# Optimization experiments

Hardware: AMD Instinct MI355X
Metric: run time of the kernel (lower is better)

Reference implementation:

```python
import jax, jax.numpy as jnp
import numpy as np

# Dims: C = 8*8*4 = 256 input channels, O = 8*8*8 = 512 output channels,
# space_rank = 4, TT ranks = (4, 16, 16).

def setup_inputs() -> dict:
    key = jax.random.key(0)
    ks = jax.random.split(key, 6)
    inp = jax.random.normal(ks[0], (32, 256, 32, 32), dtype=jnp.float32)
    # space_factor: (space_rank, 1, kH, kW)
    space_factor = jax.random.normal(ks[1], (4, 1, 3, 3), dtype=jnp.float32) * 0.3
    # factors[i]: (in_i, rank_i, rank_{i+1}, out_i)
    factor0 = jax.random.normal(ks[2], (8, 4, 16, 8), dtype=jnp.float32) * 0.1
    factor1 = jax.random.normal(ks[3], (8, 16, 16, 8), dtype=jnp.float32) * 0.08
    # last_factor: (in_last, rank_last, out_last)
    last_factor = jax.random.normal(ks[4], (4, 16, 8), dtype=jnp.float32) * 0.1
    bias = jax.random.uniform(ks[5], (512,), dtype=jnp.float32, minval=-0.02, maxval=0.02)
    return {"input": inp, "space_factor": space_factor, "factor0": factor0,
            "factor1": factor1, "last_factor": last_factor, "bias": bias}


def reference(input, space_factor, factor0, factor1, last_factor, bias):
    B, C, H, W = input.shape
    sr = space_factor.shape[0]
    # Depthwise conv: each of the C channels convolved with the same
    # `space_rank` filters (torch repeat along out-channel dim + groups=C).
    w = jnp.tile(space_factor, (C, 1, 1, 1))  # (C*sr, 1, kH, kW)
    y = jax.lax.conv_general_dilated(
        input, w, window_strides=(1, 1), padding=[(1, 1), (1, 1)],
        feature_group_count=C,
        dimension_numbers=("NCHW", "OIHW", "NCHW"))  # (B, C*sr, H', W')
    Hp, Wp = y.shape[2], y.shape[3]
    # (B, n0, n1, n2, sr, H', W') with (n0,n1,n2) = input_chanel_shape
    t = y.reshape(B, 8, 8, 4, sr, Hp, Wp)
    # Contract the tiny TT cores first (optimal order found by tn.contractors.optimal):
    # chain: (n0, n1, n2, r0, o0, o1, o2) -- only ~0.5M elements.
    chain = jnp.einsum("apqx,bqry,crz->abcpxyz", factor0, factor1, last_factor)
    # One big contraction over (n0, n1, n2, r0): effectively a GEMM
    # (B*H'*W', C*sr) x (C*sr, O).
    out = jnp.einsum("nabcphw,abcpxyz->nxyzhw", t, chain)
    out = out.reshape(B, 512, Hp, Wp)
    return out + bias[None, :, None, None]
```

## Files before the change

### kernel.cpp

```cpp
#include <hip/hip_runtime.h>

typedef unsigned short ushort_t;
typedef __attribute__((ext_vector_type(8))) short bf16x8;
typedef __attribute__((ext_vector_type(4))) float f32x4;

__device__ __forceinline__ unsigned short f2bf(float f) {
  union { float f; unsigned u; } x; x.f = f;
  unsigned r = x.u + 0x7FFFu + ((x.u >> 16) & 1u);
  return (unsigned short)(r >> 16);
}

__global__ void chain_g_kernel(const float* __restrict__ f1,
                               const float* __restrict__ lf,
                               float* __restrict__ g) {
  int idx = blockIdx.x * 256 + threadIdx.x;
  int z = idx & 7, c = (idx >> 3) & 3, y = (idx >> 5) & 7,
      q = (idx >> 8) & 15, b = idx >> 12;
  float s = 0.f;
  #pragma unroll
  for (int r = 0; r < 16; ++r)
    s += f1[((b * 16 + q) * 16 + r) * 8 + y] * lf[(c * 16 + r) * 8 + z];
  g[idx] = s;
}

__global__ void chain_kernel(const float* __restrict__ f0,
                             const float* __restrict__ g,
                             ushort_t* __restrict__ chainT) {
  int idx = blockIdx.x * 256 + threadIdx.x;
  int k = idx & 1023, o = idx >> 10;
  int p = k & 3, c = (k >> 2) & 3, b = (k >> 4) & 7, a = k >> 7;
  int z = o & 7, y = (o >> 3) & 7, x = o >> 6;
  float s = 0.f;
  #pragma unroll
  for (int q = 0; q < 16; ++q)
    s += f0[((a * 4 + p) * 16 + q) * 8 + x] *
         g[(((b * 16 + q) * 8 + y) * 4 + c) * 8 + z];
  chainT[idx] = f2bf(s);
}

#define AS1 __attribute__((address_space(1)))
#define AS3 __attribute__((address_space(3)))
#define BARRIER  __builtin_amdgcn_s_barrier()
#define LGKMCNT0 asm volatile("s_waitcnt lgkmcnt(0)" ::: "memory")
#define VMCNT0   asm volatile("s_waitcnt vmcnt(0)" ::: "memory")

__global__ __launch_bounds__(512, 2) void fused_kernel(const float* __restrict__ in,
                                                       const float* __restrict__ sf,
                                                       const ushort_t* __restrict__ chainT,
                                                       const float* __restrict__ bias,
                                                       float* __restrict__ out) {
  __shared__ __align__(16) ushort_t Bs[512 * 64];
  __shared__ __align__(16) ushort_t As[128 * 64];
  __shared__ __align__(16) float Is[2][16][6][32];

  int tid = threadIdx.x;
  int bid = blockIdx.x;
  int wg = (bid & 7) * 32 + (bid >> 3);
  int n = wg >> 3, hq = wg & 7;
  int h0 = hq * 4;

  int lane = tid & 63, wv = tid >> 6;
  int wm = (wv >> 2) * 64, wn = (wv & 3) * 128;
  int lr = lane & 15, kg = lane >> 4;
  int kph0 = ((kg * 8) ^ ((lane & 7) * 8));
  int kph1 = ((32 + kg * 8) ^ ((lane & 7) * 8));

  int srow = tid >> 3;
  int scol = ((tid & 7) ^ (srow & 7)) * 8;
  const ushort_t* sB = chainT + (size_t)srow * 1024 + scol;
  int bdst = srow * 64 + (tid & 7) * 8;

  int cw = tid & 31, hp = (tid >> 5) & 1, ch2 = tid >> 6;

  float sfr[36];
  #pragma unroll
  for (int i = 0; i < 36; ++i)
    sfr[i] = __int_as_float(__builtin_amdgcn_readfirstlane(__float_as_int(sf[i])));

  float bv[8];
  #pragma unroll
  for (int nf = 0; nf < 8; ++nf) bv[nf] = bias[wn + nf * 16 + lr];

  f32x4 acc[4][8];
  #pragma unroll
  for (int i = 0; i < 4; ++i)
    #pragma unroll
    for (int j = 0; j < 8; ++j) acc[i][j] = (f32x4){0.f, 0.f, 0.f, 0.f};

  const float* inb = in + (size_t)n * 256 * 1024;

#define STAGE_IN(kt)                                                                          \
  _Pragma("unroll")                                                                           \
  for (int i = 0; i < 2; ++i) {                                                              \
    int e = tid + i * 512;                                                                   \
    if (e < 768) {                                                                           \
      int ch = e / 48, rem = e % 48, r = rem >> 3, w4 = rem & 7;                             \
      int hh = h0 - 1 + r;                                                                   \
      float4 v = make_float4(0.f, 0.f, 0.f, 0.f);                                            \
      if (hh >= 0 && hh < 32)                                                                \
        v = *(const float4*)&inb[(size_t)((kt) * 16 + ch) * 1024 + hh * 32 + w4 * 4];        \
      *(float4*)&Is[(kt) & 1][ch][r][w4 * 4] = v;                                            \
    }                                                                                        \
  }

#define STAGE_B(kt)                                                                           \
  _Pragma("unroll")                                                                           \
  for (int l = 0; l < 8; ++l)                                                                \
    __builtin_amdgcn_global_load_lds(                                                        \
        (const AS1 void*)(sB + (size_t)l * 65536 + (kt) * 64),                               \
        (AS3 void*)&Bs[l * 4096 + bdst], 16, 0, 0);

  STAGE_IN(0)
  LGKMCNT0; BARRIER;

  for (int kt = 0; kt < 16; ++kt) {
    if (kt < 15) { STAGE_IN(kt + 1) }
    STAGE_B(kt)
    {
      int ib = kt & 1;
      #pragma unroll
      for (int b = 0; b < 2; ++b) {
        int ch = ch2 * 2 + b;
        float v[4], mL[4], mR[4];
        #pragma unroll
        for (int r = 0; r < 4; ++r) {
          float x = Is[ib][ch][hp * 2 + r][cw];
          v[r] = x;
          float up = __shfl_up(x, 1);
          float dn = __shfl_down(x, 1);
          mL[r] = (cw == 0) ? 0.f : up;
          mR[r] = (cw == 31) ? 0.f : dn;
        }
        #pragma unroll
        for (int j = 0; j < 2; ++j) {
          float s[4];
          #pragma unroll
          for (int p = 0; p < 4; ++p) {
            float a_ = 0.f;
            #pragma unroll
            for (int dr = 0; dr < 3; ++dr) {
              a_ += mL[j + dr] * sfr[p * 9 + dr * 3 + 0];
              a_ += v[j + dr]  * sfr[p * 9 + dr * 3 + 1];
              a_ += mR[j + dr] * sfr[p * 9 + dr * 3 + 2];
            }
            s[p] = a_;
          }
          unsigned lo = (unsigned)f2bf(s[0]) | ((unsigned)f2bf(s[1]) << 16);
          unsigned hi = (unsigned)f2bf(s[2]) | ((unsigned)f2bf(s[3]) << 16);
          int row = (hp * 2 + j) * 32 + cw;
          uint2 pk; pk.x = lo; pk.y = hi;
          *(uint2*)&As[row * 64 + (ch2 ^ (cw & 7)) * 8 + b * 4] = pk;
        }
      }
    }
    LGKMCNT0; VMCNT0; BARRIER;

    #pragma unroll
    for (int ks = 0; ks < 2; ++ks) {
      int kph = ks ? kph1 : kph0;
      bf16x8 af[4];
      #pragma unroll
      for (int mf = 0; mf < 4; ++mf)
        af[mf] = *(const bf16x8*)&As[(wm + mf * 16 + lr) * 64 + kph];
      #pragma unroll
      for (int ng = 0; ng < 2; ++ng) {
        bf16x8 bf4[4];
        #pragma unroll
        for (int nq = 0; nq < 4; ++nq)
          bf4[nq] = *(const bf16x8*)&Bs[(wn + ng * 64 + nq * 16 + lr) * 64 + kph];
        __builtin_amdgcn_s_setprio(1);
        #pragma unroll
        for (int mf = 0; mf < 4; ++mf)
          #pragma unroll
          for (int nq = 0; nq < 4; ++nq)
            acc[mf][ng * 4 + nq] =
                __builtin_amdgcn_mfma_f32_16x16x32_bf16(af[mf], bf4[nq], acc[mf][ng * 4 + nq], 0, 0, 0);
        __builtin_amdgcn_s_setprio(0);
      }
    }
    LGKMCNT0; BARRIER;
  }
#undef STAGE_IN
#undef STAGE_B

  #pragma unroll
  for (int mf = 0; mf < 4; ++mf)
    #pragma unroll
    for (int nf = 0; nf < 8; ++nf) {
      int mloc = hq * 128 + wm + mf * 16 + kg * 4;
      int o = wn + nf * 16 + lr;
      f32x4 vv = acc[mf][nf];
      vv[0] += bv[nf]; vv[1] += bv[nf]; vv[2] += bv[nf]; vv[3] += bv[nf];
      *(f32x4*)&out[(size_t)n * 524288 + (size_t)o * 1024 + mloc] = vv;
    }
}

extern "C" void kernel_launch(void* const* d_in, const int* in_sizes, int n_in,
                              void* d_out, int out_size, void* d_ws, size_t ws_size,
                              hipStream_t stream) {
  (void)in_sizes; (void)n_in; (void)out_size; (void)ws_size;
  const float* in   = (const float*)d_in[0];
  const float* sf   = (const float*)d_in[1];
  const float* f0   = (const float*)d_in[2];
  const float* f1   = (const float*)d_in[3];
  const float* lf   = (const float*)d_in[4];
  const float* bias = (const float*)d_in[5];
  float* out = (float*)d_out;

  char* ws = (char*)d_ws;
  ushort_t* chainT = (ushort_t*)ws;
  float*    g      = (float*)(ws + 1048576);

  hipLaunchKernelGGL(chain_g_kernel, dim3(128),  dim3(256), 0, stream, f1, lf, g);
  hipLaunchKernelGGL(chain_kernel,   dim3(2048), dim3(256), 0, stream, f0, g, chainT);
  hipLaunchKernelGGL(fused_kernel,   dim3(256),  dim3(512), 0, stream, in, sf, chainT, bias, out);
}
```

Baseline: 76.70 us.

## Software-pipeline conv staging with MFMA via double-buffered A tile and register prefetch

Restructures the main K loop into a two-stage pipeline. The A tile is double-buffered so the depthwise conv for the next K step runs right after the MFMAs of the current one. Input loads are issued into registers two steps ahead and written to LDS later, with a partial vmcnt wait so global latency stays in flight. The conv now reads halo taps from padded LDS rows instead of using lane shuffles. This adds LDS use and barrier complexity, which may reduce occupancy.

```diff
diff --git a/kernel.cpp b/kernel.cpp
--- a/kernel.cpp
+++ b/kernel.cpp
@@ -42,6 +42,7 @@
 #define AS3 __attribute__((address_space(3)))
 #define BARRIER  __builtin_amdgcn_s_barrier()
 #define LGKMCNT0 asm volatile("s_waitcnt lgkmcnt(0)" ::: "memory")
+#define VMCNT3   asm volatile("s_waitcnt vmcnt(3)" ::: "memory")
 #define VMCNT0   asm volatile("s_waitcnt vmcnt(0)" ::: "memory")
 
 __global__ __launch_bounds__(512, 2) void fused_kernel(const float* __restrict__ in,
@@ -49,9 +50,9 @@
                                                        const ushort_t* __restrict__ chainT,
                                                        const float* __restrict__ bias,
                                                        float* __restrict__ out) {
-  __shared__ __align__(16) ushort_t Bs[512 * 64];
-  __shared__ __align__(16) ushort_t As[128 * 64];
-  __shared__ __align__(16) float Is[2][16][6][32];
+  __shared__ __align__(16) ushort_t Bs[32768];
+  __shared__ __align__(16) ushort_t As[2][8192];
+  __shared__ __align__(16) float Is[6528];
 
   int tid = threadIdx.x;
   int bid = blockIdx.x;
@@ -68,9 +69,25 @@
   int srow = tid >> 3;
   int scol = ((tid & 7) ^ (srow & 7)) * 8;
   const ushort_t* sB = chainT + (size_t)srow * 1024 + scol;
-  int bdst = srow * 64 + (tid & 7) * 8;
-
-  int cw = tid & 31, hp = (tid >> 5) & 1, ch2 = tid >> 6;
+
+  int cw = tid & 31, hp = (tid >> 5) & 1, ch2 = wv;
+  int clm = (cw == 0) ? 33 : cw - 1;
+  int crp = (cw == 31) ? 32 : cw + 1;
+  int aswz = (ch2 ^ (cw & 7)) * 8;
+
+  int isrc[3], ild[3], izer[3];
+  #pragma unroll
+  for (int i = 0; i < 3; ++i) {
+    int e = tid + i * 512;
+    int ch = e / 96, rem = e % 96, r = rem >> 4, w2 = rem & 15;
+    int hh = h0 - 1 + r;
+    int hcl = hh < 0 ? 0 : (hh > 31 ? 31 : hh);
+    izer[i] = (hh < 0) | (hh > 31);
+    isrc[i] = ch * 1024 + hcl * 32 + w2 * 2;
+    ild[i]  = ch * 204 + r * 34 + w2 * 2;
+  }
+  const float* inb = in + (size_t)n * 262144;
+  float2 rin[3];
 
   float sfr[36];
   #pragma unroll
@@ -87,101 +104,122 @@
     #pragma unroll
     for (int j = 0; j < 8; ++j) acc[i][j] = (f32x4){0.f, 0.f, 0.f, 0.f};
 
-  const float* inb = in + (size_t)n * 256 * 1024;
-
-#define STAGE_IN(kt)                                                                          \
-  _Pragma("unroll")                                                                           \
-  for (int i = 0; i < 2; ++i) {                                                              \
-    int e = tid + i * 512;                                                                   \
-    if (e < 768) {                                                                           \
-      int ch = e / 48, rem = e % 48, r = rem >> 3, w4 = rem & 7;                             \
-      int hh = h0 - 1 + r;                                                                   \
-      float4 v = make_float4(0.f, 0.f, 0.f, 0.f);                                            \
-      if (hh >= 0 && hh < 32)                                                                \
-        v = *(const float4*)&inb[(size_t)((kt) * 16 + ch) * 1024 + hh * 32 + w4 * 4];        \
-      *(float4*)&Is[(kt) & 1][ch][r][w4 * 4] = v;                                            \
-    }                                                                                        \
-  }
-
-#define STAGE_B(kt)                                                                           \
-  _Pragma("unroll")                                                                           \
-  for (int l = 0; l < 8; ++l)                                                                \
-    __builtin_amdgcn_global_load_lds(                                                        \
-        (const AS1 void*)(sB + (size_t)l * 65536 + (kt) * 64),                               \
-        (AS3 void*)&Bs[l * 4096 + bdst], 16, 0, 0);
-
-  STAGE_IN(0)
+#define ISSUE_IN(KT)                                                                     \
+  _Pragma("unroll")                                                                      \
+  for (int i = 0; i < 3; ++i)                                                            \
+    rin[i] = *(const float2*)&inb[(size_t)(KT) * 16384 + isrc[i]];
+
+#define WRITE_IN(IB)                                                                     \
+  _Pragma("unroll")                                                                      \
+  for (int i = 0; i < 3; ++i) {                                                          \
+    float2 v = rin[i];                                                                   \
+    if (izer[i]) { v.x = 0.f; v.y = 0.f; }                                               \
+    *(float2*)&Is[(IB) * 3264 + ild[i]] = v;                                             \
+  }
+
+#define STAGE_B(KT)                                                                      \
+  _Pragma("unroll")                                                                      \
+  for (int l = 0; l < 8; ++l)                                                            \
+    __builtin_amdgcn_global_load_lds(                                                    \
+        (const AS1 void*)(sB + (size_t)l * 65536 + (KT) * 64),                           \
+        (AS3 void*)&Bs[l * 4096 + tid * 8], 16, 0, 0);
+
+#define CONV(IB, AB)                                                                     \
+  {                                                                                      \
+    float tap[2][4][3];                                                                  \
+    _Pragma("unroll")                                                                    \
+    for (int b = 0; b < 2; ++b) {                                                        \
+      const float* isp = &Is[(IB) * 3264 + (ch2 * 2 + b) * 204];                         \
+      _Pragma("unroll")                                                                  \
+      for (int r4 = 0; r4 < 4; ++r4) {                                                   \
+        int rb = (hp * 2 + r4) * 34;                                                     \
+        tap[b][r4][0] = isp[rb + clm];                                                   \
+        tap[b][r4][1] = isp[rb + cw];                                                    \
+        tap[b][r4][2] = isp[rb + crp];                                                   \
+      }                                                                                  \
+    }                                                                                    \
+    _Pragma("unroll")                                                                    \
+    for (int j = 0; j < 2; ++j) {                                                        \
+      unsigned pw[4];                                                                    \
+      _Pragma("unroll")                                                                  \
+      for (int b = 0; b < 2; ++b) {                                                      \
+        float s[4];                                                                      \
+        _Pragma("unroll")                                                                \
+        for (int p = 0; p < 4; ++p) {                                                    \
+          float a_ = 0.f;                                                                \
+          _Pragma("unroll")                                                              \
+          for (int dr = 0; dr < 3; ++dr)                                                 \
+            _Pragma("unroll")                                                            \
+            for (int dt = 0; dt < 3; ++dt)                                               \
+              a_ += tap[b][j + dr][dt] * sfr[p * 9 + dr * 3 + dt];                       \
+          s[p] = a_;                                                                     \
+        }                                                                                \
+        pw[b * 2 + 0] = (unsigned)f2bf(s[0]) | ((unsigned)f2bf(s[1]) << 16);             \
+        pw[b * 2 + 1] = (unsigned)f2bf(s[2]) | ((unsigned)f2bf(s[3]) << 16);             \
+      }                                                                                  \
+      uint4 pk; pk.x = pw[0]; pk.y = pw[1]; pk.z = pw[2]; pk.w = pw[3];                  \
+      int row = (hp * 2 + j) * 32 + cw;                                                  \
+      *(uint4*)&As[AB][row * 64 + aswz] = pk;                                            \
+    }                                                                                    \
+  }
+
+#define MFMA_PHASE(AB)                                                                   \
+  _Pragma("unroll")                                                                      \
+  for (int ks = 0; ks < 2; ++ks) {                                                       \
+    int kph = ks ? kph1 : kph0;                                                          \
+    bf16x8 af[4];                                                                        \
+    _Pragma("unroll")                                                                    \
+    for (int mf = 0; mf < 4; ++mf)                                                       \
+      af[mf] = *(const bf16x8*)&As[AB][(wm + mf * 16 + lr) * 64 + kph];                  \
+    _Pragma("unroll")                                                                    \
+    for (int ng = 0; ng < 2; ++ng) {                                                     \
+      bf16x8 bq[4];                                                                      \
+      _Pragma("unroll")                                                                  \
+      for (int nq = 0; nq < 4; ++nq)                                                     \
+        bq[nq] = *(const bf16x8*)&Bs[(wn + ng * 64 + nq * 16 + lr) * 64 + kph];          \
+      __builtin_amdgcn_s_setprio(1);                                                     \
+      _Pragma("unroll")                                                                  \
+      for (int mf = 0; mf < 4; ++mf)                                                     \
+        _Pragma("unroll")                                                                \
+        for (int nq = 0; nq < 4; ++nq)                                                   \
+          acc[mf][ng * 4 + nq] = __builtin_amdgcn_mfma_f32_16x16x32_bf16(                \
+              af[mf], bq[nq], acc[mf][ng * 4 + nq], 0, 0, 0);                            \
+      __builtin_amdgcn_s_setprio(0);                                                     \
+    }                                                                                    \
+  }
+
+  if (tid < 384) {
+    int bb = tid / 192, rem = tid % 192, ch = rem / 12, rr = rem % 12;
+    Is[bb * 3264 + ch * 204 + (rr >> 1) * 34 + 32 + (rr & 1)] = 0.f;
+  }
+  ISSUE_IN(0)
+  WRITE_IN(0)
+  ISSUE_IN(1)
   LGKMCNT0; BARRIER;
-
-  for (int kt = 0; kt < 16; ++kt) {
-    if (kt < 15) { STAGE_IN(kt + 1) }
-    STAGE_B(kt)
-    {
-      int ib = kt & 1;
-      #pragma unroll
-      for (int b = 0; b < 2; ++b) {
-        int ch = ch2 * 2 + b;
-        float v[4], mL[4], mR[4];
-        #pragma unroll
-        for (int r = 0; r < 4; ++r) {
-          float x = Is[ib][ch][hp * 2 + r][cw];
-          v[r] = x;
-          float up = __shfl_up(x, 1);
-          float dn = __shfl_down(x, 1);
-          mL[r] = (cw == 0) ? 0.f : up;
-          mR[r] = (cw == 31) ? 0.f : dn;
-        }
-        #pragma unroll
-        for (int j = 0; j < 2; ++j) {
-          float s[4];
-          #pragma unroll
-          for (int p = 0; p < 4; ++p) {
-            float a_ = 0.f;
-            #pragma unroll
-            for (int dr = 0; dr < 3; ++dr) {
-              a_ += mL[j + dr] * sfr[p * 9 + dr * 3 + 0];
-              a_ += v[j + dr]  * sfr[p * 9 + dr * 3 + 1];
-              a_ += mR[j + dr] * sfr[p * 9 + dr * 3 + 2];
-            }
-            s[p] = a_;
-          }
-          unsigned lo = (unsigned)f2bf(s[0]) | ((unsigned)f2bf(s[1]) << 16);
-          unsigned hi = (unsigned)f2bf(s[2]) | ((unsigned)f2bf(s[3]) << 16);
-          int row = (hp * 2 + j) * 32 + cw;
-          uint2 pk; pk.x = lo; pk.y = hi;
-          *(uint2*)&As[row * 64 + (ch2 ^ (cw & 7)) * 8 + b * 4] = pk;
-        }
-      }
+  CONV(0, 0)
+  WRITE_IN(1)
+  STAGE_B(0)
+  ISSUE_IN(2)
+  LGKMCNT0; VMCNT3; BARRIER;
+
+  #pragma unroll 1
+  for (int I = 0; I < 8; ++I) {
+    MFMA_PHASE(0)
+    CONV(1, 1)
+    if (I < 7) { WRITE_IN(0) }
+    LGKMCNT0; BARRIER;
+    STAGE_B(2 * I + 1)
+    if (I < 7) { ISSUE_IN(2 * I + 3) VMCNT3; } else { VMCNT0; }
+    BARRIER;
+    MFMA_PHASE(1)
+    if (I < 7) { CONV(0, 0) WRITE_IN(1) }
+    LGKMCNT0; BARRIER;
+    if (I < 7) {
+      STAGE_B(2 * I + 2)
+      if (I < 6) { ISSUE_IN(2 * I + 4) VMCNT3; } else { VMCNT0; }
     }
-    LGKMCNT0; VMCNT0; BARRIER;
-
-    #pragma unroll
-    for (int ks = 0; ks < 2; ++ks) {
-      int kph = ks ? kph1 : kph0;
-      bf16x8 af[4];
-      #pragma unroll
-      for (int mf = 0; mf < 4; ++mf)
-        af[mf] = *(const bf16x8*)&As[(wm + mf * 16 + lr) * 64 + kph];
-      #pragma unroll
-      for (int ng = 0; ng < 2; ++ng) {
-        bf16x8 bf4[4];
-        #pragma unroll
-        for (int nq = 0; nq < 4; ++nq)
-          bf4[nq] = *(const bf16x8*)&Bs[(wn + ng * 64 + nq * 16 + lr) * 64 + kph];
-        __builtin_amdgcn_s_setprio(1);
-        #pragma unroll
-        for (int mf = 0; mf < 4; ++mf)
-          #pragma unroll
-          for (int nq = 0; nq < 4; ++nq)
-            acc[mf][ng * 4 + nq] =
-                __builtin_amdgcn_mfma_f32_16x16x32_bf16(af[mf], bf4[nq], acc[mf][ng * 4 + nq], 0, 0, 0);
-        __builtin_amdgcn_s_setprio(0);
-      }
-    }
-    LGKMCNT0; BARRIER;
-  }
-#undef STAGE_IN
-#undef STAGE_B
+    BARRIER;
+  }
 
   #pragma unroll
   for (int mf = 0; mf < 4; ++mf)
```

Result: faster. 74.21 us (-3.2%).
